# Kernel optimization log

Hardware: AMD Instinct MI355X
Metric: run time of the kernel (lower is better)

The kernel has to match this reference:

```python
import jax, jax.numpy as jnp
import numpy as np

N, T, GX, GY, GQ = 16, 64, 256, 256, 256   # solutions, timesteps, source grid, query grid
H, D = 4, 8                                 # attention heads / head dim
SIGMA = 0.2
LY_MIN, LY_MAX = 30.0, 120.0
CU_REF, NI_REF = 0.0029, 0.0018
LX = 100.0


def setup_inputs() -> dict:
    key = jax.random.key(0)
    ks = jax.random.split(key, 7)
    lys = jax.random.uniform(ks[0], (N,), minval=40.0, maxval=110.0)
    ccu = jax.random.uniform(ks[1], (N,), minval=0.001, maxval=CU_REF)
    cni = jax.random.uniform(ks[2], (N,), minval=0.0005, maxval=NI_REF)
    params = jnp.stack([lys, ccu, cni], axis=1).astype(jnp.float32)  # [N,3] raw (Ly, C_Cu, C_Ni)
    x_grids = jnp.tile(jnp.linspace(0.0, LX, GX, dtype=jnp.float32)[None], (N, 1))      # [N,GX]
    y_grids = lys[:, None] * jnp.linspace(0.0, 1.0, GY, dtype=jnp.float32)[None]        # [N,GY]
    c1_src = jax.random.normal(ks[3], (N, T, GX, GY), dtype=jnp.float32)
    c2_src = jax.random.normal(ks[4], (N, T, GX, GY), dtype=jnp.float32)
    Wq_w = 0.1 * jax.random.normal(ks[5], (H * D, 3), dtype=jnp.float32)
    Wk_w = 0.1 * jax.random.normal(ks[6], (H * D, 3), dtype=jnp.float32)
    Wq_b = jnp.zeros((H * D,), jnp.float32)
    Wk_b = jnp.zeros((H * D,), jnp.float32)
    return dict(c1_src=c1_src, c2_src=c2_src, x_grids=x_grids, y_grids=y_grids,
                params=params, Wq_w=Wq_w, Wq_b=Wq_b, Wk_w=Wk_w, Wk_b=Wk_b,
                ly_target=jnp.float32(75.0), c_cu_target=jnp.float32(0.0029),
                c_ni_target=jnp.float32(0.0018))


def _bilinear(c, xg, yg, qx, qy):
    """Linear interp on rectilinear grid, fill_value=0 out of bounds.
    c: [T,Gx,Gy], xg: [Gx], yg: [Gy], qx/qy: [P] -> [T,P]."""
    ix = jnp.clip(jnp.searchsorted(xg, qx, side='right') - 1, 0, xg.shape[0] - 2)
    iy = jnp.clip(jnp.searchsorted(yg, qy, side='right') - 1, 0, yg.shape[0] - 2)
    x0, x1 = xg[ix], xg[ix + 1]
    y0, y1 = yg[iy], yg[iy + 1]
    fx = (qx - x0) / (x1 - x0)
    fy = (qy - y0) / (y1 - y0)
    c00 = c[:, ix, iy]
    c10 = c[:, ix + 1, iy]
    c01 = c[:, ix, iy + 1]
    c11 = c[:, ix + 1, iy + 1]
    v = ((1 - fx) * (1 - fy)) * c00 + (fx * (1 - fy)) * c10 \
        + ((1 - fx) * fy) * c01 + (fx * fy) * c11
    inb = (qx >= xg[0]) & (qx <= xg[-1]) & (qy >= yg[0]) & (qy <= yg[-1])
    return jnp.where(inb[None, :], v, 0.0)


def _forward(c1_src, c2_src, x_grids, y_grids, params, Wq_w, Wq_b, Wk_w, Wk_b,
             ly_target, c_cu_target, c_ni_target):
    # --- parameter normalization (same constants as original) ---
    p = jnp.stack([(params[:, 0] - LY_MIN) / (LY_MAX - LY_MIN),
                   params[:, 1] / CU_REF,
                   params[:, 2] / NI_REF], axis=1)                     # [N,3]
    tgt = jnp.stack([(ly_target - LY_MIN) / (LY_MAX - LY_MIN),
                     c_cu_target / CU_REF,
                     c_ni_target / NI_REF])[None, :]                   # [1,3]
    # --- tiny multi-head attention weights ---
    q = (tgt @ Wq_w.T + Wq_b).reshape(1, H, D)
    k = (p @ Wk_w.T + Wk_b).reshape(p.shape[0], H, D)
    attn = jnp.einsum('nhd,mhd->nmh', k, q) / np.sqrt(D).astype(np.float32)  # [N,1,H]
    attn_w = jax.nn.softmax(attn, axis=0).mean(axis=2).squeeze(1)            # [N]
    # --- gaussian spatial weights ---
    sw = jnp.exp(-0.5 * jnp.sum(((p - tgt) / SIGMA) ** 2, axis=1))
    sw = sw / sw.sum()
    w = attn_w * sw
    w = w / w.sum()
    w = jax.lax.stop_gradient(w)  # original detaches weights before interpolation
    # --- batched bilinear interpolation onto target grid ---
    Lx = x_grids[0, -1]
    unit = jnp.linspace(0.0, 1.0, GQ, dtype=jnp.float32)
    X, Y = jnp.meshgrid(unit * Lx, unit * ly_target, indexing='ij')    # [GQ,GQ]
    qx, qy = X.ravel(), Y.ravel()                                      # [P]
    ys = y_grids * (ly_target / params[:, 0])[:, None]                 # per-solution rescaled Y grids
    interp = jax.vmap(_bilinear, in_axes=(0, 0, 0, None, None))        # -> [N,T,P]
    c1 = jnp.einsum('n,ntp->tp', w, interp(c1_src, x_grids, ys, qx, qy)).reshape(T, GQ, GQ)
    c2 = jnp.einsum('n,ntp->tp', w, interp(c2_src, x_grids, ys, qx, qy)).reshape(T, GQ, GQ)
    # --- boundary conditions ---
    c1 = c1.at[:, :, 0].set(c_cu_target)
    c2 = c2.at[:, :, -1].set(c_ni_target)
    return jnp.stack([c1, c2]), w


def reference(c1_src, c2_src, x_grids, y_grids, params, Wq_w, Wq_b, Wk_w, Wk_b,
              ly_target, c_cu_target, c_ni_target):
    return _forward(c1_src, c2_src, x_grids, y_grids, params, Wq_w, Wq_b, Wk_w, Wk_b,
                    ly_target, c_cu_target, c_ni_target)
```

## Files before the change

### kernel.cpp

```cpp
#include <hip/hip_runtime.h>

#define N_SRC 16
#define T_DIM 64
#define GXD 256
#define GYD 256
#define GQD 256
#define HN 4
#define DN 8
#define OUT_C_ELEMS (2 * T_DIM * GQD * GQD)

#define WS_IY   0
#define WS_WY0  16384
#define WS_WY1  32768
#define WS_IX   49152
#define WS_WX0  50176
#define WS_WX1  51200

__device__ __forceinline__ float unitv(int i) {
    return (i == GQD - 1) ? 1.0f : (float)i * (1.0f / 255.0f);
}

__global__ __launch_bounds__(256) void table_kernel(
    const float* __restrict__ xg, const float* __restrict__ yg,
    const float* __restrict__ params,
    const float* __restrict__ Wq_w, const float* __restrict__ Wq_b,
    const float* __restrict__ Wk_w, const float* __restrict__ Wk_b,
    const float* __restrict__ lyt_p, const float* __restrict__ ccut_p,
    const float* __restrict__ cnit_p,
    float* __restrict__ out_w, char* __restrict__ ws)
{
    __shared__ float xg_sm[GXD];
    __shared__ float ys_sm[N_SRC][GYD];
    __shared__ float w_sm[N_SRC];

    const int tid = threadIdx.x;
    const float lyt = *lyt_p;

    xg_sm[tid] = xg[tid];
    #pragma unroll
    for (int n = 0; n < N_SRC; ++n) {
        float s = lyt / params[n * 3 + 0];
        ys_sm[n][tid] = yg[n * GYD + tid] * s;
    }

    if (tid == 0) {
        const float ccut = *ccut_p, cnit = *cnit_p;
        float tgt[3];
        tgt[0] = (lyt - 30.0f) / 90.0f;
        tgt[1] = ccut / 0.0029f;
        tgt[2] = cnit / 0.0018f;
        float q[HN * DN];
        for (int hd = 0; hd < HN * DN; ++hd)
            q[hd] = tgt[0] * Wq_w[hd * 3 + 0] + tgt[1] * Wq_w[hd * 3 + 1] + tgt[2] * Wq_w[hd * 3 + 2] + Wq_b[hd];
        float p[N_SRC][3];
        float attn[N_SRC][HN];
        for (int n = 0; n < N_SRC; ++n) {
            p[n][0] = (params[n * 3 + 0] - 30.0f) / 90.0f;
            p[n][1] = params[n * 3 + 1] / 0.0029f;
            p[n][2] = params[n * 3 + 2] / 0.0018f;
            for (int h = 0; h < HN; ++h) {
                float acc = 0.0f;
                for (int d = 0; d < DN; ++d) {
                    int hd = h * DN + d;
                    float kv = p[n][0] * Wk_w[hd * 3 + 0] + p[n][1] * Wk_w[hd * 3 + 1] + p[n][2] * Wk_w[hd * 3 + 2] + Wk_b[hd];
                    acc += kv * q[hd];
                }
                attn[n][h] = acc / sqrtf(8.0f);
            }
        }
        float aw[N_SRC];
        for (int n = 0; n < N_SRC; ++n) aw[n] = 0.0f;
        for (int h = 0; h < HN; ++h) {
            float m = attn[0][h];
            for (int n = 1; n < N_SRC; ++n) m = fmaxf(m, attn[n][h]);
            float e[N_SRC], s = 0.0f;
            for (int n = 0; n < N_SRC; ++n) { e[n] = expf(attn[n][h] - m); s += e[n]; }
            for (int n = 0; n < N_SRC; ++n) aw[n] += e[n] / s;
        }
        for (int n = 0; n < N_SRC; ++n) aw[n] *= (1.0f / (float)HN);
        float sw[N_SRC], ss = 0.0f;
        for (int n = 0; n < N_SRC; ++n) {
            float d0 = (p[n][0] - tgt[0]) / 0.2f;
            float d1 = (p[n][1] - tgt[1]) / 0.2f;
            float d2 = (p[n][2] - tgt[2]) / 0.2f;
            sw[n] = expf(-0.5f * (d0 * d0 + d1 * d1 + d2 * d2));
            ss += sw[n];
        }
        float w[N_SRC], wsum = 0.0f;
        for (int n = 0; n < N_SRC; ++n) { w[n] = aw[n] * (sw[n] / ss); wsum += w[n]; }
        for (int n = 0; n < N_SRC; ++n) {
            float wf = w[n] / wsum;
            w_sm[n] = wf;
            out_w[n] = wf;
        }
    }
    __syncthreads();

    int*   iy_tab  = (int*)  (ws + WS_IY);
    float* wy0_tab = (float*)(ws + WS_WY0);
    float* wy1_tab = (float*)(ws + WS_WY1);
    int*   ix_tab  = (int*)  (ws + WS_IX);
    float* wx0_tab = (float*)(ws + WS_WX0);
    float* wx1_tab = (float*)(ws + WS_WX1);

    const int j = tid;
    const float qy = unitv(j) * lyt;
    #pragma unroll
    for (int n = 0; n < N_SRC; ++n) {
        int lo = 0, hi = GYD;
        while (lo < hi) { int mid = (lo + hi) >> 1; if (ys_sm[n][mid] <= qy) lo = mid + 1; else hi = mid; }
        int idx = lo - 1;
        idx = idx < 0 ? 0 : (idx > GYD - 2 ? GYD - 2 : idx);
        float y0 = ys_sm[n][idx], y1 = ys_sm[n][idx + 1];
        float fy = (qy - y0) / (y1 - y0);
        float vy = (qy >= ys_sm[n][0] && qy <= ys_sm[n][GYD - 1]) ? 1.0f : 0.0f;
        float wn = w_sm[n] * vy;
        iy_tab [n * GQD + j] = idx;
        wy0_tab[n * GQD + j] = wn * (1.0f - fy);
        wy1_tab[n * GQD + j] = wn * fy;
    }

    const float Lx = xg_sm[GXD - 1];
    const float qx = unitv(tid) * Lx;
    int lo = 0, hi = GXD;
    while (lo < hi) { int mid = (lo + hi) >> 1; if (xg_sm[mid] <= qx) lo = mid + 1; else hi = mid; }
    int ixi = lo - 1;
    ixi = ixi < 0 ? 0 : (ixi > GXD - 2 ? GXD - 2 : ixi);
    const float x0 = xg_sm[ixi], x1 = xg_sm[ixi + 1];
    const float fx = (qx - x0) / (x1 - x0);
    const float vx = (qx >= xg_sm[0] && qx <= xg_sm[GXD - 1]) ? 1.0f : 0.0f;
    ix_tab [tid] = ixi;
    wx0_tab[tid] = vx * (1.0f - fx);
    wx1_tab[tid] = vx * fx;
}

__global__ __launch_bounds__(256) void fused_kernel(
    const float* __restrict__ c1, const float* __restrict__ c2,
    const float* __restrict__ ccut_p, const float* __restrict__ cnit_p,
    const char* __restrict__ ws, float* __restrict__ out)
{
    const int i = blockIdx.x;
    const int t = blockIdx.y;
    const int j = threadIdx.x;

    const int*   iy_tab  = (const int*)  (ws + WS_IY);
    const float* wy0_tab = (const float*)(ws + WS_WY0);
    const float* wy1_tab = (const float*)(ws + WS_WY1);

    const int   ixi = ((const int*)  (ws + WS_IX)) [i];
    const float wx0 = ((const float*)(ws + WS_WX0))[i];
    const float wx1 = ((const float*)(ws + WS_WX1))[i];

    float a10 = 0.0f, a11 = 0.0f, a20 = 0.0f, a21 = 0.0f;

    #pragma unroll 4
    for (int n = 0; n < N_SRC; ++n) {
        const int   iy  = iy_tab [n * GQD + j];
        const float wy0 = wy0_tab[n * GQD + j];
        const float wy1 = wy1_tab[n * GQD + j];
        const int base = ((n * T_DIM + t) * GXD + ixi) * GYD + iy;
        const float e00 = c1[base],       e01 = c1[base + 1];
        const float e10 = c1[base + GYD], e11 = c1[base + GYD + 1];
        a10 += wy0 * e00 + wy1 * e01;
        a11 += wy0 * e10 + wy1 * e11;
        const float f00 = c2[base],       f01 = c2[base + 1];
        const float f10 = c2[base + GYD], f11 = c2[base + GYD + 1];
        a20 += wy0 * f00 + wy1 * f01;
        a21 += wy0 * f10 + wy1 * f11;
    }

    float o1 = wx0 * a10 + wx1 * a11;
    float o2 = wx0 * a20 + wx1 * a21;
    if (j == 0)       o1 = *ccut_p;
    if (j == GQD - 1) o2 = *cnit_p;
    out[(t * GQD + i) * GQD + j] = o1;
    out[((T_DIM + t) * GQD + i) * GQD + j] = o2;
}

extern "C" void kernel_launch(void* const* d_in, const int* in_sizes, int n_in,
                              void* d_out, int out_size, void* d_ws, size_t ws_size,
                              hipStream_t stream) {
    const float* c1     = (const float*)d_in[0];
    const float* c2     = (const float*)d_in[1];
    const float* xg     = (const float*)d_in[2];
    const float* yg     = (const float*)d_in[3];
    const float* params = (const float*)d_in[4];
    const float* Wq_w   = (const float*)d_in[5];
    const float* Wq_b   = (const float*)d_in[6];
    const float* Wk_w   = (const float*)d_in[7];
    const float* Wk_b   = (const float*)d_in[8];
    const float* lyt    = (const float*)d_in[9];
    const float* ccut   = (const float*)d_in[10];
    const float* cnit   = (const float*)d_in[11];
    float* out = (float*)d_out;
    float* out_w = out + OUT_C_ELEMS;
    char* ws = (char*)d_ws;

    table_kernel<<<1, 256, 0, stream>>>(xg, yg, params, Wq_w, Wq_b, Wk_w, Wk_b,
                                        lyt, ccut, cnit, out_w, ws);
    dim3 grid(GQD, T_DIM);
    fused_kernel<<<grid, 256, 0, stream>>>(c1, c2, ccut, cnit, ws, out);
}
```

Baseline: 685.8 us.

## Tile 16 query rows per block, stage source rows in LDS with double buffering

Each block now handles 16 query rows for one timestep. For each solution and field, it copies the contiguous span of source x-rows those queries need into LDS with global_load_lds, double-buffered across the 32 planes, and reuses each y-interpolated row for adjacent query rows. The aim is to remove the redundant, scattered global gathers of the old one-row-per-block kernel, where neighbouring blocks reread the same source rows. The cost is fewer blocks (1024), about 37KB of LDS per block, and a full waitcnt plus barrier per plane. Row spans are clamped to 18, so a wider span would be silently wrong.

```diff
diff --git a/kernel.cpp b/kernel.cpp
--- a/kernel.cpp
+++ b/kernel.cpp
@@ -7,6 +7,8 @@
 #define GQD 256
 #define HN 4
 #define DN 8
+#define TI 16
+#define MAXROWS 18
 #define OUT_C_ELEMS (2 * T_DIM * GQD * GQD)
 
 #define WS_IY   0
@@ -134,47 +136,134 @@
     wx1_tab[tid] = vx * fx;
 }
 
+__device__ __forceinline__ void gl_lds16(const float4* g, float4* l) {
+    __builtin_amdgcn_global_load_lds(
+        (const __attribute__((address_space(1))) void*)g,
+        (__attribute__((address_space(3))) void*)l, 16, 0, 0);
+}
+
 __global__ __launch_bounds__(256) void fused_kernel(
     const float* __restrict__ c1, const float* __restrict__ c2,
     const float* __restrict__ ccut_p, const float* __restrict__ cnit_p,
     const char* __restrict__ ws, float* __restrict__ out)
 {
-    const int i = blockIdx.x;
+    __shared__ float buf[2][MAXROWS * GYD];
+    __shared__ int   ixb_sm[TI];
+    __shared__ float wx0_sm[TI], wx1_sm[TI];
+
+    const int tid = threadIdx.x;
+    const int j = tid;
+    const int i0 = blockIdx.x * TI;
     const int t = blockIdx.y;
-    const int j = threadIdx.x;
 
     const int*   iy_tab  = (const int*)  (ws + WS_IY);
     const float* wy0_tab = (const float*)(ws + WS_WY0);
     const float* wy1_tab = (const float*)(ws + WS_WY1);
 
-    const int   ixi = ((const int*)  (ws + WS_IX)) [i];
-    const float wx0 = ((const float*)(ws + WS_WX0))[i];
-    const float wx1 = ((const float*)(ws + WS_WX1))[i];
-
-    float a10 = 0.0f, a11 = 0.0f, a20 = 0.0f, a21 = 0.0f;
-
-    #pragma unroll 4
-    for (int n = 0; n < N_SRC; ++n) {
-        const int   iy  = iy_tab [n * GQD + j];
-        const float wy0 = wy0_tab[n * GQD + j];
-        const float wy1 = wy1_tab[n * GQD + j];
-        const int base = ((n * T_DIM + t) * GXD + ixi) * GYD + iy;
-        const float e00 = c1[base],       e01 = c1[base + 1];
-        const float e10 = c1[base + GYD], e11 = c1[base + GYD + 1];
-        a10 += wy0 * e00 + wy1 * e01;
-        a11 += wy0 * e10 + wy1 * e11;
-        const float f00 = c2[base],       f01 = c2[base + 1];
-        const float f10 = c2[base + GYD], f11 = c2[base + GYD + 1];
-        a20 += wy0 * f00 + wy1 * f01;
-        a21 += wy0 * f10 + wy1 * f11;
-    }
-
-    float o1 = wx0 * a10 + wx1 * a11;
-    float o2 = wx0 * a20 + wx1 * a21;
-    if (j == 0)       o1 = *ccut_p;
-    if (j == GQD - 1) o2 = *cnit_p;
-    out[(t * GQD + i) * GQD + j] = o1;
-    out[((T_DIM + t) * GQD + i) * GQD + j] = o2;
+    if (tid < TI) {
+        ixb_sm[tid] = ((const int*)  (ws + WS_IX)) [i0 + tid];
+        wx0_sm[tid] = ((const float*)(ws + WS_WX0))[i0 + tid];
+        wx1_sm[tid] = ((const float*)(ws + WS_WX1))[i0 + tid];
+    }
+    __syncthreads();
+
+    const int x0r = ixb_sm[0];
+    int nrows = ixb_sm[TI - 1] + 2 - x0r;
+    nrows = nrows > MAXROWS ? MAXROWS : nrows;
+    const int chunks4 = nrows * (GYD / 4);
+
+    int   r0r[TI];
+    float wx0r[TI], wx1r[TI];
+    #pragma unroll
+    for (int ii = 0; ii < TI; ++ii) {
+        r0r[ii]  = ixb_sm[ii] - x0r;
+        wx0r[ii] = wx0_sm[ii];
+        wx1r[ii] = wx1_sm[ii];
+    }
+
+    float acc1[TI], acc2[TI];
+    #pragma unroll
+    for (int ii = 0; ii < TI; ++ii) { acc1[ii] = 0.0f; acc2[ii] = 0.0f; }
+
+    auto plane_src = [&](int p) -> const float4* {
+        const int n = p >> 1;
+        const float* base = (p & 1) ? c2 : c1;
+        return (const float4*)(base + (((size_t)n * T_DIM + t) * GXD + x0r) * GYD);
+    };
+
+    {
+        const float4* g = plane_src(0);
+        float4* l = (float4*)&buf[0][0];
+        #pragma unroll
+        for (int k = 0; k < 5; ++k) {
+            int c = tid + k * 256;
+            if (c < chunks4) gl_lds16(g + c, l + c);
+        }
+    }
+
+    int   iyv = 0;
+    float wy0v = 0.0f, wy1v = 0.0f;
+
+    for (int p = 0; p < 2 * N_SRC; ++p) {
+        __builtin_amdgcn_s_waitcnt(0);
+        __syncthreads();
+
+        if (p + 1 < 2 * N_SRC) {
+            const float4* g = plane_src(p + 1);
+            float4* l = (float4*)&buf[(p + 1) & 1][0];
+            #pragma unroll
+            for (int k = 0; k < 5; ++k) {
+                int c = tid + k * 256;
+                if (c < chunks4) gl_lds16(g + c, l + c);
+            }
+        }
+
+        const int n = p >> 1;
+        if ((p & 1) == 0) {
+            iyv  = iy_tab [n * GQD + j];
+            wy0v = wy0_tab[n * GQD + j];
+            wy1v = wy1_tab[n * GQD + j];
+        }
+
+        const float* B = &buf[p & 1][0];
+        int loaded = -1;
+        float vm1 = 0.0f, vcur = 0.0f;
+        if ((p & 1) == 0) {
+            #pragma unroll
+            for (int ii = 0; ii < TI; ++ii) {
+                const int r1 = r0r[ii] + 1;
+                while (loaded < r1) {
+                    ++loaded;
+                    vm1 = vcur;
+                    vcur = wy0v * B[loaded * GYD + iyv] + wy1v * B[loaded * GYD + iyv + 1];
+                }
+                acc1[ii] += wx0r[ii] * vm1 + wx1r[ii] * vcur;
+            }
+        } else {
+            #pragma unroll
+            for (int ii = 0; ii < TI; ++ii) {
+                const int r1 = r0r[ii] + 1;
+                while (loaded < r1) {
+                    ++loaded;
+                    vm1 = vcur;
+                    vcur = wy0v * B[loaded * GYD + iyv] + wy1v * B[loaded * GYD + iyv + 1];
+                }
+                acc2[ii] += wx0r[ii] * vm1 + wx1r[ii] * vcur;
+            }
+        }
+    }
+
+    const float ccut = *ccut_p, cnit = *cnit_p;
+    #pragma unroll
+    for (int ii = 0; ii < TI; ++ii) {
+        const int i = i0 + ii;
+        float o1 = acc1[ii];
+        float o2 = acc2[ii];
+        if (j == 0)       o1 = ccut;
+        if (j == GQD - 1) o2 = cnit;
+        out[(t * GQD + i) * GQD + j] = o1;
+        out[((T_DIM + t) * GQD + i) * GQD + j] = o2;
+    }
 }
 
 extern "C" void kernel_launch(void* const* d_in, const int* in_sizes, int n_in,
@@ -198,6 +287,6 @@
 
     table_kernel<<<1, 256, 0, stream>>>(xg, yg, params, Wq_w, Wq_b, Wk_w, Wk_b,
                                         lyt, ccut, cnit, out_w, ws);
-    dim3 grid(GQD, T_DIM);
+    dim3 grid(GQD / TI, T_DIM);
     fused_kernel<<<grid, 256, 0, stream>>>(c1, c2, ccut, cnit, ws, out);
 }
```

Result: faster. 630.8 us (-8.0%).
